# Kernel optimization log

Measured on AMD Instinct MI355X. Metric: run time of the kernel, lower is better.

## Reference

```python
import jax, jax.numpy as jnp
import numpy as np

N, E, G, DIM = 100000, 1600000, 64, 128
BN_EPS = 1e-5


def setup_inputs() -> dict:
    key = jax.random.key(0)
    ks = jax.random.split(key, 20)
    inp = {
        "x": jax.random.normal(ks[0], (N, DIM), jnp.float32),
        "edge_attr": jax.random.normal(ks[1], (E, DIM), jnp.float32),
        "u": jax.random.normal(ks[2], (G, DIM), jnp.float32),
        "edge_index": jax.random.randint(ks[3], (2, E), 0, N, jnp.int32),
        "batch": jnp.sort(jax.random.randint(ks[4], (N,), 0, G, jnp.int32)),
    }
    # MLP params: layer 0 is Linear(3*DIM, DIM), layers 1,2 are Linear(DIM, DIM)
    def xavier(k, shape):
        fan_in, fan_out = shape[1], shape[0]
        lim = jnp.sqrt(6.0 / (fan_in + fan_out))
        return jax.random.uniform(k, shape, jnp.float32, -lim, lim)
    inp["W0"] = xavier(ks[5], (DIM, 3 * DIM)); inp["b0"] = jnp.zeros((DIM,), jnp.float32)
    inp["W1"] = xavier(ks[6], (DIM, DIM));     inp["b1"] = jnp.zeros((DIM,), jnp.float32)
    inp["W2"] = xavier(ks[7], (DIM, DIM));     inp["b2"] = jnp.zeros((DIM,), jnp.float32)
    for i in range(3):
        inp[f"g{i}"] = jnp.ones((DIM,), jnp.float32)   # BN gamma
        inp[f"bt{i}"] = jnp.zeros((DIM,), jnp.float32)  # BN beta
    return inp


def _bn(h, gamma, beta):
    # training-mode BatchNorm1d: batch mean, biased variance
    mu = jnp.mean(h, axis=0)
    var = jnp.var(h, axis=0)
    return (h - mu) * jax.lax.rsqrt(var + BN_EPS) * gamma + beta


def reference(x, edge_attr, u, W0, b0, W1, b1, W2, b2,
              g0, bt0, g1, bt1, g2, bt2, edge_index, batch):
    n = x.shape[0]
    src = edge_index[0]
    # scatter_mean(edge_attr, src) -> [N, DIM]
    sums = jax.ops.segment_sum(edge_attr, src, num_segments=n)
    cnt = jax.ops.segment_sum(jnp.ones((edge_attr.shape[0],), edge_attr.dtype),
                              src, num_segments=n)
    v_e = sums / jnp.maximum(cnt, 1.0)[:, None]
    out = jnp.concatenate([x, v_e, u[batch]], axis=1)  # [N, 3*DIM]
    for W, b, g, bt in ((W0, b0, g0, bt0), (W1, b1, g1, bt1), (W2, b2, g2, bt2)):
        out = jax.nn.relu(out @ W.T + b)
        out = _bn(out, g, bt)
        # dropout_rate = 0.0 -> identity
    return out
```

## Files before the change

### kernel.cpp

```cpp
#include <hip/hip_runtime.h>

#define DIMF 128
#define CAP 128

typedef __bf16 bf16x8 __attribute__((ext_vector_type(8)));
typedef float f32x4 __attribute__((ext_vector_type(4)));

__device__ __forceinline__ unsigned short f2bf(float f) {
    union { float f; unsigned u; } v; v.f = f;
    unsigned r = v.u + 0x7FFFu + ((v.u >> 16) & 1u);
    return (unsigned short)(r >> 16);
}
__device__ __forceinline__ float bf2f(unsigned short h) {
    union { unsigned u; float f; } v; v.u = ((unsigned)h) << 16; return v.f;
}

__global__ __launch_bounds__(256) void k_zero_wconv(int* __restrict__ zbase, int zints,
                                                    const float* __restrict__ W, unsigned short* __restrict__ Wb,
                                                    int n4) {
    int idx = blockIdx.x * 256 + threadIdx.x;
    int z0 = idx * 2;
    if (z0 + 1 < zints) {
        *reinterpret_cast<int2*>(zbase + z0) = int2{0, 0};
    } else if (z0 < zints) {
        zbase[z0] = 0;
    }
    if (idx < n4) {
        float4 v = *reinterpret_cast<const float4*>(W + (size_t)idx * 4);
        ushort4 o = { f2bf(v.x), f2bf(v.y), f2bf(v.z), f2bf(v.w) };
        *reinterpret_cast<ushort4*>(Wb + (size_t)idx * 4) = o;
    }
}

__global__ __launch_bounds__(256) void k_fillb(const int* __restrict__ src, int* __restrict__ cnt,
                                               int* __restrict__ order, int E) {
    int e = blockIdx.x * 256 + threadIdx.x;
    if (e < E) {
        int s = src[e];
        int p = atomicAdd(&cnt[s], 1);
        if (p < CAP) order[(size_t)s * CAP + p] = e;
    }
}

__global__ __launch_bounds__(256) void k_gather(const float* __restrict__ ea, const int* __restrict__ order,
                                                const int* __restrict__ cnt,
                                                unsigned short* __restrict__ ve, int n) {
    int node = blockIdx.x * 4 + (threadIdx.x >> 6);
    if (node >= n) return;
    int lane = threadIdx.x & 63;
    int half = lane >> 5;
    int l32 = lane & 31;
    int c = cnt[node];
    if (c > CAP) c = CAP;
    size_t base = (size_t)node * CAP;

    int id0 = (lane < c) ? order[base + lane] : 0;
    int id1 = (c > 64 && lane < c - 64) ? order[base + 64 + lane] : 0;

    int m  = (c > half) ? ((c - half + 1) >> 1) : 0;
    int mu = (c + 1) >> 1;

#define EID(t) ({ int j_ = half + 2 * (t); \
                  (j_ < 64) ? __shfl(id0, j_, 64) : __shfl(id1, j_ - 64, 64); })
#define LDR(eid) __builtin_nontemporal_load(reinterpret_cast<const f32x4*>(ea + (size_t)(eid) * DIMF) + l32)

    f32x4 s = {0.f, 0.f, 0.f, 0.f};
    f32x4 cur[4], nxt[4];
    int tb = mu >> 2;
    if (tb > 0) {
#pragma unroll
        for (int k = 0; k < 4; ++k) cur[k] = LDR(EID(k));
        for (int b = 1; b < tb; ++b) {
#pragma unroll
            for (int k = 0; k < 4; ++k) nxt[k] = LDR(EID(b * 4 + k));
#pragma unroll
            for (int k = 0; k < 4; ++k) {
                int t = (b - 1) * 4 + k;
                if (t < m) s += cur[k];
                cur[k] = nxt[k];
            }
        }
#pragma unroll
        for (int k = 0; k < 4; ++k) {
            int t = (tb - 1) * 4 + k;
            if (t < m) s += cur[k];
        }
    }
    for (int t = tb * 4; t < mu; ++t) {
        f32x4 v = LDR(EID(t));
        if (t < m) s += v;
    }
#undef EID
#undef LDR

    s[0] += __shfl_xor(s[0], 32, 64);
    s[1] += __shfl_xor(s[1], 32, 64);
    s[2] += __shfl_xor(s[2], 32, 64);
    s[3] += __shfl_xor(s[3], 32, 64);

    if (lane < 32) {
        float inv = 1.0f / (float)(c > 1 ? c : 1);
        ushort4 o = { f2bf(s[0] * inv), f2bf(s[1] * inv), f2bf(s[2] * inv), f2bf(s[3] * inv) };
        *reinterpret_cast<ushort4*>(ve + (size_t)node * DIMF + l32 * 4) = o;
    }
}

#define BM 128

__global__ __launch_bounds__(1024, 8) void k_gemm0(const float* __restrict__ x,
                                                   const unsigned short* __restrict__ ve,
                                                   const float* __restrict__ u,
                                                   const int* __restrict__ batch,
                                                   const unsigned short* __restrict__ W,
                                                   const float* __restrict__ bias,
                                                   unsigned short* __restrict__ H,
                                                   float* __restrict__ st, int rows) {
    __shared__ __align__(16) unsigned short lA[BM][136];
    __shared__ __align__(16) unsigned short lB[DIMF][136];
    __shared__ float sm[DIMF], sq[DIMF];
    __shared__ int sbatch[BM];
    int tid = threadIdx.x;
    int row0 = blockIdx.x * BM;
    if (tid < DIMF) { sm[tid] = 0.f; sq[tid] = 0.f; }
    if (tid < BM) {
        int gr = row0 + tid;
        sbatch[tid] = (gr < rows) ? batch[gr] : 0;
    }

    int lane = tid & 63, wave = tid >> 6;
    int wm = wave >> 2, wn = wave & 3;
    int l15 = lane & 15, l4 = lane >> 4;
    f32x4 acc[2][2] = {};

    int fr = tid >> 5, fc = (tid & 31) * 4;
    int hr = tid >> 4, hc = (tid & 15) * 8;

#pragma unroll
    for (int chunk = 0; chunk < 3; ++chunk) {
        if (chunk == 0) {
#pragma unroll
            for (int i = 0; i < 4; ++i) {
                int r = fr + i * 32;
                int gr = row0 + r;
                float4 v = (gr < rows) ? *reinterpret_cast<const float4*>(x + (size_t)gr * DIMF + fc)
                                       : float4{0.f, 0.f, 0.f, 0.f};
                ushort4 o2 = { f2bf(v.x), f2bf(v.y), f2bf(v.z), f2bf(v.w) };
                *reinterpret_cast<ushort4*>(&lA[r][fc]) = o2;
            }
        } else if (chunk == 1) {
#pragma unroll
            for (int i = 0; i < 2; ++i) {
                int r = hr + i * 64;
                int gr = row0 + r;
                uint4 v = (gr < rows) ? *reinterpret_cast<const uint4*>(ve + (size_t)gr * DIMF + hc)
                                      : uint4{0u, 0u, 0u, 0u};
                *reinterpret_cast<uint4*>(&lA[r][hc]) = v;
            }
        } else {
#pragma unroll
            for (int i = 0; i < 4; ++i) {
                int r = fr + i * 32;
                int gr = row0 + r;
                int b = sbatch[r];
                float4 v = (gr < rows) ? *reinterpret_cast<const float4*>(u + (size_t)b * DIMF + fc)
                                       : float4{0.f, 0.f, 0.f, 0.f};
                ushort4 o2 = { f2bf(v.x), f2bf(v.y), f2bf(v.z), f2bf(v.w) };
                *reinterpret_cast<ushort4*>(&lA[r][fc]) = o2;
            }
        }
#pragma unroll
        for (int i = 0; i < 2; ++i) {
            int r = hr + i * 64;
            uint4 v = *reinterpret_cast<const uint4*>(W + (size_t)r * 384 + chunk * 128 + hc);
            *reinterpret_cast<uint4*>(&lB[r][hc]) = v;
        }
        __syncthreads();
#pragma unroll
        for (int ks = 0; ks < 4; ++ks) {
            bf16x8 af[2], bfr[2];
#pragma unroll
            for (int mi = 0; mi < 2; ++mi)
                af[mi] = *reinterpret_cast<const bf16x8*>(&lA[wm * 32 + mi * 16 + l15][ks * 32 + l4 * 8]);
#pragma unroll
            for (int ni = 0; ni < 2; ++ni)
                bfr[ni] = *reinterpret_cast<const bf16x8*>(&lB[wn * 32 + ni * 16 + l15][ks * 32 + l4 * 8]);
#pragma unroll
            for (int mi = 0; mi < 2; ++mi)
#pragma unroll
                for (int ni = 0; ni < 2; ++ni)
                    acc[mi][ni] = __builtin_amdgcn_mfma_f32_16x16x32_bf16(af[mi], bfr[ni], acc[mi][ni], 0, 0, 0);
        }
        __syncthreads();
    }

#pragma unroll
    for (int mi = 0; mi < 2; ++mi)
#pragma unroll
        for (int ni = 0; ni < 2; ++ni) {
            int c = wn * 32 + ni * 16 + l15;
            float s = 0.f, q = 0.f;
#pragma unroll
            for (int i = 0; i < 4; ++i) {
                int r = row0 + wm * 32 + mi * 16 + l4 * 4 + i;
                if (r < rows) {
                    float z = acc[mi][ni][i] + bias[c];
                    z = fmaxf(z, 0.f);
                    H[(size_t)r * DIMF + c] = f2bf(z);
                    s += z; q += z * z;
                }
            }
            atomicAdd(&sm[c], s);
            atomicAdd(&sq[c], q);
        }
    __syncthreads();
    if (tid < DIMF) { atomicAdd(&st[tid], sm[tid]); atomicAdd(&st[DIMF + tid], sq[tid]); }
}

__global__ __launch_bounds__(1024, 8) void k_gemmF(const unsigned short* __restrict__ A,
                                                   const float* __restrict__ W,
                                                   const float* __restrict__ bn,
                                                   const float* __restrict__ stp,
                                                   const float* __restrict__ g,
                                                   const float* __restrict__ bt,
                                                   unsigned short* __restrict__ H,
                                                   float* __restrict__ st, int rows) {
    const int K = 128;
    __shared__ __align__(16) unsigned short lA[BM][136];
    __shared__ __align__(16) unsigned short lB[DIMF][136];
    __shared__ float sS[DIMF], sT[DIMF], bb[DIMF], sm[DIMF], sq[DIMF];
    int tid = threadIdx.x;
    int row0 = blockIdx.x * BM;

    if (tid < DIMF) {
        float invn = 1.0f / (float)rows;
        float mu = stp[tid] * invn;
        float var = stp[DIMF + tid] * invn - mu * mu;
        var = var > 0.f ? var : 0.f;
        float sc = rsqrtf(var + 1e-5f) * g[tid];
        sS[tid] = sc;
        sT[tid] = bt[tid] - mu * sc;
        sm[tid] = 0.f; sq[tid] = 0.f;
    }

    int hr = tid >> 4, hc = (tid & 15) * 8;
#pragma unroll
    for (int i = 0; i < 2; ++i) {
        int r = hr + i * 64;
        int gr = row0 + r;
        uint4 v = (gr < rows) ? *reinterpret_cast<const uint4*>(A + (size_t)gr * K + hc)
                              : uint4{0u, 0u, 0u, 0u};
        *reinterpret_cast<uint4*>(&lA[r][hc]) = v;
    }
    __syncthreads();

    int fr = tid >> 5, fc = (tid & 31) * 4;
#pragma unroll
    for (int it = 0; it < 4; ++it) {
        int r = fr + it * 32;
        float4 w = *reinterpret_cast<const float4*>(W + (size_t)r * K + fc);
        ushort4 ob = { f2bf(w.x * sS[fc]), f2bf(w.y * sS[fc + 1]),
                       f2bf(w.z * sS[fc + 2]), f2bf(w.w * sS[fc + 3]) };
        *reinterpret_cast<ushort4*>(&lB[r][fc]) = ob;
        float p = w.x * sT[fc] + w.y * sT[fc + 1] + w.z * sT[fc + 2] + w.w * sT[fc + 3];
#pragma unroll
        for (int m = 16; m > 0; m >>= 1) p += __shfl_xor(p, m, 32);
        if ((tid & 31) == 0) bb[r] = bn[r] + p;
    }
    __syncthreads();

    int lane = tid & 63, wave = tid >> 6;
    int wm = wave >> 2, wn = wave & 3;
    int l15 = lane & 15, l4 = lane >> 4;
    f32x4 acc[2][2] = {};

#pragma unroll
    for (int ks = 0; ks < 4; ++ks) {
        bf16x8 af[2], bfr[2];
#pragma unroll
        for (int mi = 0; mi < 2; ++mi)
            af[mi] = *reinterpret_cast<const bf16x8*>(&lA[wm * 32 + mi * 16 + l15][ks * 32 + l4 * 8]);
#pragma unroll
        for (int ni = 0; ni < 2; ++ni)
            bfr[ni] = *reinterpret_cast<const bf16x8*>(&lB[wn * 32 + ni * 16 + l15][ks * 32 + l4 * 8]);
#pragma unroll
        for (int mi = 0; mi < 2; ++mi)
#pragma unroll
            for (int ni = 0; ni < 2; ++ni)
                acc[mi][ni] = __builtin_amdgcn_mfma_f32_16x16x32_bf16(af[mi], bfr[ni], acc[mi][ni], 0, 0, 0);
    }

#pragma unroll
    for (int mi = 0; mi < 2; ++mi)
#pragma unroll
        for (int ni = 0; ni < 2; ++ni) {
            int c = wn * 32 + ni * 16 + l15;
            float s = 0.f, q = 0.f;
#pragma unroll
            for (int i = 0; i < 4; ++i) {
                int r = row0 + wm * 32 + mi * 16 + l4 * 4 + i;
                if (r < rows) {
                    float z = acc[mi][ni][i] + bb[c];
                    z = fmaxf(z, 0.f);
                    H[(size_t)r * DIMF + c] = f2bf(z);
                    s += z; q += z * z;
                }
            }
            atomicAdd(&sm[c], s);
            atomicAdd(&sq[c], q);
        }
    __syncthreads();
    if (tid < DIMF) { atomicAdd(&st[tid], sm[tid]); atomicAdd(&st[DIMF + tid], sq[tid]); }
}

__global__ __launch_bounds__(256) void k_final(const unsigned short* __restrict__ H, const float* __restrict__ st,
                                               const float* __restrict__ g, const float* __restrict__ bt,
                                               float* __restrict__ out, int n) {
    int idx = blockIdx.x * 256 + threadIdx.x;
    if (idx >= n * 32) return;
    int r = idx >> 5, q = (idx & 31) * 4;
    float invn = 1.0f / (float)n;
    ushort4 h = *reinterpret_cast<const ushort4*>(H + (size_t)r * DIMF + q);
    float hv[4] = { bf2f(h.x), bf2f(h.y), bf2f(h.z), bf2f(h.w) };
    float ov[4];
#pragma unroll
    for (int k = 0; k < 4; ++k) {
        int c = q + k;
        float mu = st[c] * invn;
        float var = st[DIMF + c] * invn - mu * mu;
        var = var > 0.f ? var : 0.f;
        float sc = rsqrtf(var + 1e-5f) * g[c];
        ov[k] = hv[k] * sc + (bt[c] - mu * sc);
    }
    float4 o = { ov[0], ov[1], ov[2], ov[3] };
    *reinterpret_cast<float4*>(out + (size_t)r * DIMF + q) = o;
}

extern "C" void kernel_launch(void* const* d_in, const int* in_sizes, int n_in,
                              void* d_out, int out_size, void* d_ws, size_t ws_size,
                              hipStream_t stream) {
    const float* x   = (const float*)d_in[0];
    const float* ea  = (const float*)d_in[1];
    const float* u   = (const float*)d_in[2];
    const int* eidx  = (const int*)d_in[3];
    const int* batch = (const int*)d_in[4];
    const float* W0  = (const float*)d_in[5];
    const float* b0  = (const float*)d_in[6];
    const float* W1  = (const float*)d_in[7];
    const float* b1  = (const float*)d_in[8];
    const float* W2  = (const float*)d_in[9];
    const float* b2  = (const float*)d_in[10];
    const float* g0  = (const float*)d_in[11];
    const float* bt0 = (const float*)d_in[12];
    const float* g1  = (const float*)d_in[13];
    const float* bt1 = (const float*)d_in[14];
    const float* g2  = (const float*)d_in[15];
    const float* bt2 = (const float*)d_in[16];

    int N = in_sizes[0] / DIMF;
    int E = in_sizes[1] / DIMF;
    const int* src = eidx;

    char* base = (char*)d_ws;
    size_t o = 0;
    auto alloc = [&](size_t sz) { size_t p = o; o = (o + sz + 255) & ~(size_t)255; return p; };
    size_t off_cnt   = alloc((size_t)N * 4);
    size_t off_st    = alloc(3 * 256 * 4);
    size_t off_order = alloc((size_t)N * CAP * 4);
    size_t off_W0b   = alloc((size_t)DIMF * 384 * 2);
    size_t off_ve    = alloc((size_t)N * DIMF * 2);
    size_t off_h0    = alloc((size_t)N * DIMF * 2);
    size_t off_h1    = alloc((size_t)N * DIMF * 2);
    size_t off_h2    = alloc((size_t)N * DIMF * 2);

    int* cnt        = (int*)(base + off_cnt);
    float* st       = (float*)(base + off_st);
    int* order      = (int*)(base + off_order);
    unsigned short* W0b = (unsigned short*)(base + off_W0b);
    unsigned short* ve  = (unsigned short*)(base + off_ve);
    unsigned short* h0  = (unsigned short*)(base + off_h0);
    unsigned short* h1  = (unsigned short*)(base + off_h1);
    unsigned short* h2  = (unsigned short*)(base + off_h2);
    float* outp = (float*)d_out;

    int zints = (int)((off_st + 3 * 256 * 4) / 4);
    int EB = (E + 255) / 256;
    int NQ = (N * 32 + 255) / 256;
    int GB = (N + BM - 1) / BM;
    int GG = (N + 3) / 4;

    k_zero_wconv<<<256, 256, 0, stream>>>((int*)base, zints, W0, W0b, DIMF * 384 / 4);
    k_fillb<<<EB, 256, 0, stream>>>(src, cnt, order, E);
    k_gather<<<GG, 256, 0, stream>>>(ea, order, cnt, ve, N);

    k_gemm0<<<GB, 1024, 0, stream>>>(x, ve, u, batch, W0b, b0, h0, st, N);
    k_gemmF<<<GB, 1024, 0, stream>>>(h0, W1, b1, st, g0, bt0, h1, st + 256, N);
    k_gemmF<<<GB, 1024, 0, stream>>>(h1, W2, b2, st + 256, g1, bt1, h2, st + 512, N);
    k_final<<<NQ, 256, 0, stream>>>(h2, st + 512, g2, bt2, outp, N);
}
```

Before: 507.8 us.

## Fuse edge scatter-mean gather into first GEMM kernel, dropping ve buffer

Removes the separate gather kernel and computes the per-node edge mean directly inside k_gemm0. Each wave handles 8 rows and writes the bf16 mean straight into the LDS A tile, and the v_e chunk of the GEMM runs first. This avoids writing and re-reading the intermediate ve array and saves one kernel launch. In exchange the gather now runs inside a 1024-thread GEMM block with a shallower prefetch depth of 2, which may lower memory-level parallelism on the 800MB edge_attr stream.

Result: faster. 491.7 us (-3.2%).

```diff
diff --git a/kernel.cpp b/kernel.cpp
--- a/kernel.cpp
+++ b/kernel.cpp
@@ -42,73 +42,12 @@
     }
 }
 
-__global__ __launch_bounds__(256) void k_gather(const float* __restrict__ ea, const int* __restrict__ order,
-                                                const int* __restrict__ cnt,
-                                                unsigned short* __restrict__ ve, int n) {
-    int node = blockIdx.x * 4 + (threadIdx.x >> 6);
-    if (node >= n) return;
-    int lane = threadIdx.x & 63;
-    int half = lane >> 5;
-    int l32 = lane & 31;
-    int c = cnt[node];
-    if (c > CAP) c = CAP;
-    size_t base = (size_t)node * CAP;
-
-    int id0 = (lane < c) ? order[base + lane] : 0;
-    int id1 = (c > 64 && lane < c - 64) ? order[base + 64 + lane] : 0;
-
-    int m  = (c > half) ? ((c - half + 1) >> 1) : 0;
-    int mu = (c + 1) >> 1;
-
-#define EID(t) ({ int j_ = half + 2 * (t); \
-                  (j_ < 64) ? __shfl(id0, j_, 64) : __shfl(id1, j_ - 64, 64); })
-#define LDR(eid) __builtin_nontemporal_load(reinterpret_cast<const f32x4*>(ea + (size_t)(eid) * DIMF) + l32)
-
-    f32x4 s = {0.f, 0.f, 0.f, 0.f};
-    f32x4 cur[4], nxt[4];
-    int tb = mu >> 2;
-    if (tb > 0) {
-#pragma unroll
-        for (int k = 0; k < 4; ++k) cur[k] = LDR(EID(k));
-        for (int b = 1; b < tb; ++b) {
-#pragma unroll
-            for (int k = 0; k < 4; ++k) nxt[k] = LDR(EID(b * 4 + k));
-#pragma unroll
-            for (int k = 0; k < 4; ++k) {
-                int t = (b - 1) * 4 + k;
-                if (t < m) s += cur[k];
-                cur[k] = nxt[k];
-            }
-        }
-#pragma unroll
-        for (int k = 0; k < 4; ++k) {
-            int t = (tb - 1) * 4 + k;
-            if (t < m) s += cur[k];
-        }
-    }
-    for (int t = tb * 4; t < mu; ++t) {
-        f32x4 v = LDR(EID(t));
-        if (t < m) s += v;
-    }
-#undef EID
-#undef LDR
-
-    s[0] += __shfl_xor(s[0], 32, 64);
-    s[1] += __shfl_xor(s[1], 32, 64);
-    s[2] += __shfl_xor(s[2], 32, 64);
-    s[3] += __shfl_xor(s[3], 32, 64);
-
-    if (lane < 32) {
-        float inv = 1.0f / (float)(c > 1 ? c : 1);
-        ushort4 o = { f2bf(s[0] * inv), f2bf(s[1] * inv), f2bf(s[2] * inv), f2bf(s[3] * inv) };
-        *reinterpret_cast<ushort4*>(ve + (size_t)node * DIMF + l32 * 4) = o;
-    }
-}
-
 #define BM 128
 
 __global__ __launch_bounds__(1024, 8) void k_gemm0(const float* __restrict__ x,
-                                                   const unsigned short* __restrict__ ve,
+                                                   const float* __restrict__ ea,
+                                                   const int* __restrict__ order,
+                                                   const int* __restrict__ cnt,
                                                    const float* __restrict__ u,
                                                    const int* __restrict__ batch,
                                                    const unsigned short* __restrict__ W,
@@ -130,43 +69,102 @@
     int lane = tid & 63, wave = tid >> 6;
     int wm = wave >> 2, wn = wave & 3;
     int l15 = lane & 15, l4 = lane >> 4;
-    f32x4 acc[2][2] = {};
+    int half = lane >> 5, l32 = lane & 31;
 
     int fr = tid >> 5, fc = (tid & 31) * 4;
     int hr = tid >> 4, hc = (tid & 15) * 8;
 
-#pragma unroll
-    for (int chunk = 0; chunk < 3; ++chunk) {
-        if (chunk == 0) {
-#pragma unroll
-            for (int i = 0; i < 4; ++i) {
-                int r = fr + i * 32;
-                int gr = row0 + r;
-                float4 v = (gr < rows) ? *reinterpret_cast<const float4*>(x + (size_t)gr * DIMF + fc)
-                                       : float4{0.f, 0.f, 0.f, 0.f};
-                ushort4 o2 = { f2bf(v.x), f2bf(v.y), f2bf(v.z), f2bf(v.w) };
-                *reinterpret_cast<ushort4*>(&lA[r][fc]) = o2;
+#pragma unroll 1
+    for (int i = 0; i < 8; ++i) {
+        int r = wave * 8 + i;
+        int node = row0 + r;
+        f32x4 s = {0.f, 0.f, 0.f, 0.f};
+        int c = 0;
+        if (node < rows) {
+            c = cnt[node];
+            if (c > CAP) c = CAP;
+            size_t nb = (size_t)node * CAP;
+            int id0 = (lane < c) ? order[nb + lane] : 0;
+            int id1 = (c > 64 && lane < c - 64) ? order[nb + 64 + lane] : 0;
+            int m  = (c > half) ? ((c - half + 1) >> 1) : 0;
+            int mu = (c + 1) >> 1;
+
+#define EID(t) ({ int j_ = half + 2 * (t); \
+                  (j_ < 64) ? __shfl(id0, j_, 64) : __shfl(id1, j_ - 64, 64); })
+#define LDR(eid) __builtin_nontemporal_load(reinterpret_cast<const f32x4*>(ea + (size_t)(eid) * DIMF) + l32)
+
+            f32x4 cur0, cur1, nxt0, nxt1;
+            int tb = mu >> 1;
+            if (tb > 0) {
+                cur0 = LDR(EID(0));
+                cur1 = LDR(EID(1));
+                for (int b = 1; b < tb; ++b) {
+                    nxt0 = LDR(EID(2 * b));
+                    nxt1 = LDR(EID(2 * b + 1));
+                    if (2 * b - 2 < m) s += cur0;
+                    if (2 * b - 1 < m) s += cur1;
+                    cur0 = nxt0; cur1 = nxt1;
+                }
+                if (2 * tb - 2 < m) s += cur0;
+                if (2 * tb - 1 < m) s += cur1;
             }
-        } else if (chunk == 1) {
-#pragma unroll
-            for (int i = 0; i < 2; ++i) {
-                int r = hr + i * 64;
-                int gr = row0 + r;
-                uint4 v = (gr < rows) ? *reinterpret_cast<const uint4*>(ve + (size_t)gr * DIMF + hc)
-                                      : uint4{0u, 0u, 0u, 0u};
-                *reinterpret_cast<uint4*>(&lA[r][hc]) = v;
+            for (int t = tb * 2; t < mu; ++t) {
+                f32x4 v = LDR(EID(t));
+                if (t < m) s += v;
             }
-        } else {
-#pragma unroll
-            for (int i = 0; i < 4; ++i) {
-                int r = fr + i * 32;
-                int gr = row0 + r;
-                int b = sbatch[r];
-                float4 v = (gr < rows) ? *reinterpret_cast<const float4*>(u + (size_t)b * DIMF + fc)
-                                       : float4{0.f, 0.f, 0.f, 0.f};
-                ushort4 o2 = { f2bf(v.x), f2bf(v.y), f2bf(v.z), f2bf(v.w) };
-                *reinterpret_cast<ushort4*>(&lA[r][fc]) = o2;
-            }
+#undef EID
+#undef LDR
+            s[0] += __shfl_xor(s[0], 32, 64);
+            s[1] += __shfl_xor(s[1], 32, 64);
+            s[2] += __shfl_xor(s[2], 32, 64);
+            s[3] += __shfl_xor(s[3], 32, 64);
+        }
+        if (lane < 32) {
+            float inv = 1.0f / (float)(c > 1 ? c : 1);
+            ushort4 o = { f2bf(s[0] * inv), f2bf(s[1] * inv), f2bf(s[2] * inv), f2bf(s[3] * inv) };
+            *reinterpret_cast<ushort4*>(&lA[r][l32 * 4]) = o;
+        }
+    }
+
+    f32x4 acc[2][2] = {};
+
+#pragma unroll
+    for (int i = 0; i < 2; ++i) {
+        int r = hr + i * 64;
+        uint4 v = *reinterpret_cast<const uint4*>(W + (size_t)r * 384 + 128 + hc);
+        *reinterpret_cast<uint4*>(&lB[r][hc]) = v;
+    }
+    __syncthreads();
+#pragma unroll
+    for (int ks = 0; ks < 4; ++ks) {
+        bf16x8 af[2], bfr[2];
+#pragma unroll
+        for (int mi = 0; mi < 2; ++mi)
+            af[mi] = *reinterpret_cast<const bf16x8*>(&lA[wm * 32 + mi * 16 + l15][ks * 32 + l4 * 8]);
+#pragma unroll
+        for (int ni = 0; ni < 2; ++ni)
+            bfr[ni] = *reinterpret_cast<const bf16x8*>(&lB[wn * 32 + ni * 16 + l15][ks * 32 + l4 * 8]);
+#pragma unroll
+        for (int mi = 0; mi < 2; ++mi)
+#pragma unroll
+            for (int ni = 0; ni < 2; ++ni)
+                acc[mi][ni] = __builtin_amdgcn_mfma_f32_16x16x32_bf16(af[mi], bfr[ni], acc[mi][ni], 0, 0, 0);
+    }
+    __syncthreads();
+
+#pragma unroll
+    for (int pass = 0; pass < 2; ++pass) {
+        int chunk = pass * 2;
+#pragma unroll
+        for (int i = 0; i < 4; ++i) {
+            int r = fr + i * 32;
+            int gr = row0 + r;
+            const float* srcp = (pass == 0) ? (x + (size_t)gr * DIMF + fc)
+                                            : (u + (size_t)sbatch[r] * DIMF + fc);
+            float4 v = (gr < rows) ? *reinterpret_cast<const float4*>(srcp)
+                                   : float4{0.f, 0.f, 0.f, 0.f};
+            ushort4 o2 = { f2bf(v.x), f2bf(v.y), f2bf(v.z), f2bf(v.w) };
+            *reinterpret_cast<ushort4*>(&lA[r][fc]) = o2;
         }
 #pragma unroll
         for (int i = 0; i < 2; ++i) {
@@ -367,7 +365,6 @@
     size_t off_st    = alloc(3 * 256 * 4);
     size_t off_order = alloc((size_t)N * CAP * 4);
     size_t off_W0b   = alloc((size_t)DIMF * 384 * 2);
-    size_t off_ve    = alloc((size_t)N * DIMF * 2);
     size_t off_h0    = alloc((size_t)N * DIMF * 2);
     size_t off_h1    = alloc((size_t)N * DIMF * 2);
     size_t off_h2    = alloc((size_t)N * DIMF * 2);
@@ -376,7 +373,6 @@
     float* st       = (float*)(base + off_st);
     int* order      = (int*)(base + off_order);
     unsigned short* W0b = (unsigned short*)(base + off_W0b);
-    unsigned short* ve  = (unsigned short*)(base + off_ve);
     unsigned short* h0  = (unsigned short*)(base + off_h0);
     unsigned short* h1  = (unsigned short*)(base + off_h1);
     unsigned short* h2  = (unsigned short*)(base + off_h2);
@@ -386,13 +382,11 @@
     int EB = (E + 255) / 256;
     int NQ = (N * 32 + 255) / 256;
     int GB = (N + BM - 1) / BM;
-    int GG = (N + 3) / 4;
 
     k_zero_wconv<<<256, 256, 0, stream>>>((int*)base, zints, W0, W0b, DIMF * 384 / 4);
     k_fillb<<<EB, 256, 0, stream>>>(src, cnt, order, E);
-    k_gather<<<GG, 256, 0, stream>>>(ea, order, cnt, ve, N);
-
-    k_gemm0<<<GB, 1024, 0, stream>>>(x, ve, u, batch, W0b, b0, h0, st, N);
+
+    k_gemm0<<<GB, 1024, 0, stream>>>(x, ea, order, cnt, u, batch, W0b, b0, h0, st, N);
     k_gemmF<<<GB, 1024, 0, stream>>>(h0, W1, b1, st, g0, bt0, h1, st + 256, N);
     k_gemmF<<<GB, 1024, 0, stream>>>(h1, W2, b2, st + 256, g1, bt1, h2, st + 512, N);
     k_final<<<NQ, 256, 0, stream>>>(h2, st + 512, g2, bt2, outp, N);
```
